# Kernel tuning notes

Measured on AMD Instinct MI355X. Metric: run time of the kernel, lower is better.

The kernel has to match this reference:

```python
import jax, jax.numpy as jnp
import numpy as np

EPS = 1e-8  # torch F.cosine_similarity norm clamp


def setup_inputs() -> dict:
    key = jax.random.key(0)
    k1, k2, k3, k4 = jax.random.split(key, 4)
    B, N, M, D, T = 8, 4096, 2048, 512, 2
    return {
        "features": jax.random.normal(k1, (B, N, D), dtype=jnp.float32),
        "text": jax.random.normal(k2, (T, M, D), dtype=jnp.float32),
        "W": jax.random.normal(k3, (D, D), dtype=jnp.float32) * 0.02,
        "b": jax.random.normal(k4, (D,), dtype=jnp.float32) * 0.02,
    }


def reference(features, text, W, b):
    # features: [B, N, D] (output of the extractor), text: [T, M, D]
    B, N, D = features.shape
    f1 = jnp.einsum("bnd,de->bne", features, W) + b  # linear_layer(features)
    t1 = text[1]  # [M, D]; expanded across batch (row 1 per original code)

    # cosine similarity over last dim without materializing [B, N, M, D]
    fn = f1 / jnp.maximum(jnp.linalg.norm(f1, axis=-1, keepdims=True), EPS)
    tn = t1 / jnp.maximum(jnp.linalg.norm(t1, axis=-1, keepdims=True), EPS)
    sim = jnp.einsum("bnd,md->bnm", fn, tn)  # [B, N, M]

    e = jnp.exp(sim)
    w = e / jnp.sum(e, axis=1, keepdims=True)  # normalize over N (dim=1)

    # features_t [B,D,N] @ w [B,N,M] -> [B,D,M] -> transpose -> [B,M,D]
    fm = jnp.einsum("bnd,bnm->bmd", features, w)

    t1b = jnp.broadcast_to(t1[None, :, :], (B,) + t1.shape)  # [B, M, D]
    combine_feature = jnp.concatenate([fm, t1b], axis=2)  # [B, M, 2D]
    return combine_feature
```

## Files before the change

### kernel.cpp

```cpp
#include <hip/hip_runtime.h>

#define B_SZ 8
#define N_SZ 4096
#define M_SZ 2048
#define D_SZ 512

typedef __attribute__((ext_vector_type(8))) short bf16x8;
typedef __attribute__((ext_vector_type(4))) float f32x4;
typedef __attribute__((address_space(1))) const void* gptr1;
typedef __attribute__((address_space(3))) void* lptr3;

__device__ __forceinline__ unsigned short f2bf(float x) {
    unsigned int u = __builtin_bit_cast(unsigned int, x);
    u += 0x7fffu + ((u >> 16) & 1u);
    return (unsigned short)(u >> 16);
}
__device__ __forceinline__ float bf2f(unsigned short u) {
    unsigned int x = ((unsigned int)u) << 16;
    return __builtin_bit_cast(float, x);
}

__device__ __forceinline__ void bt_mainloop(
    const unsigned short* __restrict__ A, const unsigned short* __restrict__ Bt,
    int lda, int ldb, int rowBase, int colBase, int K,
    unsigned short* As, unsigned short* Bs, f32x4 acc[4][4])
{
    const int tid  = threadIdx.x;
    const int lane = tid & 63;
    const int w    = tid >> 6;
    const int wr   = (w >> 1) * 64;
    const int wc   = (w & 1) * 64;
    const int lr   = lane & 15;
    const int kq   = lane >> 4;

    const int srow0 = w * 16 + (lane >> 2);
    const int skk   = (lane & 3) * 8;

    for (int k0 = 0; k0 < K; k0 += 32) {
#pragma unroll
        for (int j = 0; j < 2; ++j) {
            const unsigned short* ga = A  + (size_t)(rowBase + srow0 + j * 64) * lda + (k0 + skk);
            const unsigned short* gb = Bt + (size_t)(colBase + srow0 + j * 64) * ldb + (k0 + skk);
            __builtin_amdgcn_global_load_lds((gptr1)ga, (lptr3)(As + (j * 4 + w) * 512), 16, 0, 0);
            __builtin_amdgcn_global_load_lds((gptr1)gb, (lptr3)(Bs + (j * 4 + w) * 512), 16, 0, 0);
        }
        asm volatile("s_waitcnt vmcnt(0)" ::: "memory");
        __syncthreads();

        bf16x8 af[4], bq[4];
#pragma unroll
        for (int i = 0; i < 4; ++i) {
            af[i] = *(const bf16x8*)(As + (wr + i * 16 + lr) * 32 + kq * 8);
            bq[i] = *(const bf16x8*)(Bs + (wc + i * 16 + lr) * 32 + kq * 8);
        }
#pragma unroll
        for (int mi = 0; mi < 4; ++mi)
#pragma unroll
            for (int ni = 0; ni < 4; ++ni)
                acc[mi][ni] = __builtin_amdgcn_mfma_f32_16x16x32_bf16(af[mi], bq[ni], acc[mi][ni], 0, 0, 0);
        __syncthreads();
    }
}

__global__ __launch_bounds__(256) void prep_tn_k(
    const float* __restrict__ text, unsigned short* __restrict__ tn,
    float* __restrict__ out, float* __restrict__ L, float* __restrict__ SS)
{
    const int m = blockIdx.x;
    const int t = threadIdx.x;
    const float* t1 = text + (size_t)M_SZ * D_SZ;
    float2 v = ((const float2*)(t1 + (size_t)m * D_SZ))[t];
    float s = v.x * v.x + v.y * v.y;
#pragma unroll
    for (int off = 32; off > 0; off >>= 1) s += __shfl_down(s, off);
    __shared__ float partial[4];
    if ((t & 63) == 0) partial[t >> 6] = s;
    __syncthreads();
    float norm = sqrtf(partial[0] + partial[1] + partial[2] + partial[3]);
    norm = fmaxf(norm, 1e-8f);
    const float inv = 1.f / norm;
    ushort2 pk; pk.x = f2bf(v.x * inv); pk.y = f2bf(v.y * inv);
    ((ushort2*)(tn + (size_t)m * D_SZ))[t] = pk;
#pragma unroll
    for (int b = 0; b < B_SZ; ++b)
        ((float2*)(out + ((size_t)(b * M_SZ + m)) * (2 * D_SZ) + D_SZ))[t] = v;
    if (m < 64) L[m * 256 + t] = 0.f;
    if (m < 128) SS[m * 256 + t] = 0.f;
}

__global__ __launch_bounds__(256) void prep_w_k(
    const float* __restrict__ W, unsigned short* __restrict__ Wt)
{
    const int dt = blockIdx.x, et = blockIdx.y;
    const int t = threadIdx.x;
    __shared__ unsigned short tile[64][72];
    const int rr = t >> 4;
    const int cc = (t & 15) * 4;
#pragma unroll
    for (int p = 0; p < 4; ++p) {
        const int d = p * 16 + rr;
        const float4 v = *(const float4*)(W + (size_t)(dt * 64 + d) * D_SZ + et * 64 + cc);
        tile[d][cc] = f2bf(v.x); tile[d][cc + 1] = f2bf(v.y);
        tile[d][cc + 2] = f2bf(v.z); tile[d][cc + 3] = f2bf(v.w);
    }
    __syncthreads();
#pragma unroll
    for (int p = 0; p < 4; ++p) {
        const int e = p * 16 + rr;
        ushort4 pk;
        pk.x = tile[cc][e]; pk.y = tile[cc + 1][e]; pk.z = tile[cc + 2][e]; pk.w = tile[cc + 3][e];
        *(ushort4*)(Wt + (size_t)(et * 64 + e) * D_SZ + dt * 64 + cc) = pk;
    }
}

__global__ __launch_bounds__(256) void convert_feat_k(
    const float* __restrict__ feat, unsigned short* __restrict__ V,
    unsigned short* __restrict__ Vt)
{
    const int nt = blockIdx.x, dt = blockIdx.y, b = blockIdx.z;
    const int t = threadIdx.x;
    __shared__ unsigned short tile[64][72];
    const int rr = t >> 4;
    const int cc = (t & 15) * 4;
#pragma unroll
    for (int p = 0; p < 4; ++p) {
        const int r = p * 16 + rr;
        const size_t grow = (size_t)(b * N_SZ + nt * 64 + r);
        const float4 v = *(const float4*)(feat + grow * D_SZ + dt * 64 + cc);
        ushort4 pk; pk.x = f2bf(v.x); pk.y = f2bf(v.y); pk.z = f2bf(v.z); pk.w = f2bf(v.w);
        *(ushort4*)(V + grow * D_SZ + dt * 64 + cc) = pk;
        tile[r][cc] = pk.x; tile[r][cc + 1] = pk.y; tile[r][cc + 2] = pk.z; tile[r][cc + 3] = pk.w;
    }
    __syncthreads();
#pragma unroll
    for (int p = 0; p < 4; ++p) {
        const int d = p * 16 + rr;
        ushort4 pk;
        pk.x = tile[cc][d]; pk.y = tile[cc + 1][d]; pk.z = tile[cc + 2][d]; pk.w = tile[cc + 3][d];
        *(ushort4*)(Vt + ((size_t)(b * D_SZ + dt * 64 + d)) * N_SZ + nt * 64 + cc) = pk;
    }
}

__global__ __launch_bounds__(256) void gemm1_k(
    const unsigned short* __restrict__ V, const unsigned short* __restrict__ Wt,
    const float* __restrict__ bias, unsigned short* __restrict__ f1b,
    float* __restrict__ SS)
{
    __shared__ unsigned short As[128 * 32];
    __shared__ unsigned short Bs[128 * 32];
    f32x4 acc[4][4];
#pragma unroll
    for (int i = 0; i < 4; ++i)
#pragma unroll
        for (int j = 0; j < 4; ++j) acc[i][j] = (f32x4){0.f, 0.f, 0.f, 0.f};
    const int tid = threadIdx.x, lane = tid & 63, w = tid >> 6;
    const int wr = (w >> 1) * 64, wc = (w & 1) * 64, lr = lane & 15, kq = lane >> 4;

    const int rowBase = blockIdx.x * 128;
    const int colBase = blockIdx.y * 128;
    bt_mainloop(V, Wt, D_SZ, D_SZ, rowBase, colBase, D_SZ, As, Bs, acc);

#pragma unroll
    for (int mi = 0; mi < 4; ++mi) {
        const int r0 = rowBase + wr + mi * 16 + kq * 4;
        float s[4] = {0.f, 0.f, 0.f, 0.f};
#pragma unroll
        for (int ni = 0; ni < 4; ++ni) {
            const int c = colBase + wc + ni * 16 + lr;
            const float bv = bias[c];
#pragma unroll
            for (int r = 0; r < 4; ++r) {
                const float v = acc[mi][ni][r] + bv;
                f1b[(size_t)(r0 + r) * D_SZ + c] = f2bf(v);
                s[r] += v * v;
            }
        }
#pragma unroll
        for (int off = 1; off <= 8; off <<= 1)
#pragma unroll
            for (int r = 0; r < 4; ++r) s[r] += __shfl_xor(s[r], off);
        if (lr == 0) {
#pragma unroll
            for (int r = 0; r < 4; ++r) atomicAdd(&SS[r0 + r], s[r]);
        }
    }
}

__global__ __launch_bounds__(128) void normalize_k(
    const unsigned short* __restrict__ f1b, const float* __restrict__ SS,
    unsigned short* __restrict__ fn)
{
    const int row = blockIdx.x;
    const int t = threadIdx.x;
    const float norm = fmaxf(sqrtf(SS[row]), 1e-8f);
    const float inv = 1.f / norm;
    ushort4 v = ((const ushort4*)(f1b + (size_t)row * D_SZ))[t];
    ushort4 o;
    o.x = f2bf(bf2f(v.x) * inv); o.y = f2bf(bf2f(v.y) * inv);
    o.z = f2bf(bf2f(v.z) * inv); o.w = f2bf(bf2f(v.w) * inv);
    ((ushort4*)(fn + (size_t)row * D_SZ))[t] = o;
}

__global__ __launch_bounds__(256) void gemm2_k(
    const unsigned short* __restrict__ fn, const unsigned short* __restrict__ tn,
    unsigned short* __restrict__ E, float* __restrict__ L)
{
    __shared__ unsigned short smem[128 * 136];
    unsigned short* As = smem;
    unsigned short* Bs = smem + 4096;
    f32x4 acc[4][4];
#pragma unroll
    for (int i = 0; i < 4; ++i)
#pragma unroll
        for (int j = 0; j < 4; ++j) acc[i][j] = (f32x4){0.f, 0.f, 0.f, 0.f};
    const int tid = threadIdx.x, lane = tid & 63, w = tid >> 6;
    const int wr = (w >> 1) * 64, wc = (w & 1) * 64, lr = lane & 15, kq = lane >> 4;

    const int lin = blockIdx.x;
    const int xcd = lin & 7, slot = lin >> 3;
    const int mt = slot & 15;
    const int rt = (slot >> 4) * 8 + xcd;
    const int rowBase = rt * 128;
    const int colBase = mt * 128;

    bt_mainloop(fn, tn, D_SZ, D_SZ, rowBase, colBase, D_SZ, As, Bs, acc);

    const int b  = rowBase >> 12;
    const int nb = rowBase & 4095;
    unsigned short* Eb = E + (size_t)b * M_SZ * N_SZ;
    unsigned short* P = smem;

#pragma unroll
    for (int ni = 0; ni < 4; ++ni) {
        const int mm = wc + ni * 16 + lr;
        float p = 0.f;
#pragma unroll
        for (int mi = 0; mi < 4; ++mi) {
            const int nn0 = wr + mi * 16 + kq * 4;
            const float e0 = __expf(acc[mi][ni][0]);
            const float e1 = __expf(acc[mi][ni][1]);
            const float e2 = __expf(acc[mi][ni][2]);
            const float e3 = __expf(acc[mi][ni][3]);
            ushort4 pk; pk.x = f2bf(e0); pk.y = f2bf(e1); pk.z = f2bf(e2); pk.w = f2bf(e3);
            *(ushort4*)(P + mm * 136 + nn0) = pk;
            p += (e0 + e1) + (e2 + e3);
        }
        p += __shfl_down(p, 16);
        p += __shfl_down(p, 32);
        if (lane < 16) atomicAdd(&L[b * M_SZ + colBase + mm], p);
    }
    __syncthreads();

    const int tr = tid >> 4;
    const int tc = (tid & 15) * 8;
#pragma unroll
    for (int j = 0; j < 8; ++j) {
        const int mm = j * 16 + tr;
        bf16x8 v = *(const bf16x8*)(P + mm * 136 + tc);
        *(bf16x8*)(Eb + (size_t)(colBase + mm) * N_SZ + nb + tc) = v;
    }
}

__global__ __launch_bounds__(256) void gemm3_k(
    const unsigned short* __restrict__ E, const unsigned short* __restrict__ Vt,
    const float* __restrict__ L, float* __restrict__ out)
{
    __shared__ unsigned short As[128 * 32];
    __shared__ unsigned short Bs[128 * 32];
    f32x4 acc[4][4];
#pragma unroll
    for (int i = 0; i < 4; ++i)
#pragma unroll
        for (int j = 0; j < 4; ++j) acc[i][j] = (f32x4){0.f, 0.f, 0.f, 0.f};
    const int tid = threadIdx.x, lane = tid & 63, w = tid >> 6;
    const int wr = (w >> 1) * 64, wc = (w & 1) * 64, lr = lane & 15, kq = lane >> 4;

    const int b = blockIdx.z;
    const int rowBase = blockIdx.x * 128;
    const int colBase = blockIdx.y * 128;
    const unsigned short* Ab = E + (size_t)b * M_SZ * N_SZ;
    const unsigned short* Bb = Vt + (size_t)b * D_SZ * N_SZ;
    bt_mainloop(Ab, Bb, N_SZ, N_SZ, rowBase, colBase, N_SZ, As, Bs, acc);

#pragma unroll
    for (int mi = 0; mi < 4; ++mi) {
        const int r0 = rowBase + wr + mi * 16 + kq * 4;
        float invl[4];
#pragma unroll
        for (int r = 0; r < 4; ++r) invl[r] = 1.f / L[b * M_SZ + r0 + r];
#pragma unroll
        for (int ni = 0; ni < 4; ++ni) {
            const int d = colBase + wc + ni * 16 + lr;
#pragma unroll
            for (int r = 0; r < 4; ++r)
                out[((size_t)(b * M_SZ + r0 + r)) * (2 * D_SZ) + d] = acc[mi][ni][r] * invl[r];
        }
    }
}

extern "C" void kernel_launch(void* const* d_in, const int* in_sizes, int n_in,
                              void* d_out, int out_size, void* d_ws, size_t ws_size,
                              hipStream_t stream) {
    const float* features = (const float*)d_in[0];
    const float* text     = (const float*)d_in[1];
    const float* W        = (const float*)d_in[2];
    const float* bias     = (const float*)d_in[3];
    float* out = (float*)d_out;
    char* ws = (char*)d_ws;

    unsigned short* fn  = (unsigned short*)(ws + 0);
    unsigned short* tn  = (unsigned short*)(ws + 33554432);
    unsigned short* Wt  = (unsigned short*)(ws + 35651584);
    unsigned short* V   = (unsigned short*)(ws + 36175872);
    unsigned short* Vt  = (unsigned short*)(ws + 69730304);
    float*          L   = (float*)(ws + 103284736);
    float*          SS  = (float*)(ws + 103350272);
    unsigned short* E   = (unsigned short*)(ws + 103481344);
    unsigned short* f1b = (unsigned short*)(ws + 103481344);

    hipLaunchKernelGGL(prep_tn_k, dim3(M_SZ), dim3(256), 0, stream, text, tn, out, L, SS);
    hipLaunchKernelGGL(prep_w_k, dim3(8, 8), dim3(256), 0, stream, W, Wt);
    hipLaunchKernelGGL(convert_feat_k, dim3(64, 8, 8), dim3(256), 0, stream, features, V, Vt);
    hipLaunchKernelGGL(gemm1_k, dim3(256, 4), dim3(256), 0, stream, V, Wt, bias, f1b, SS);
    hipLaunchKernelGGL(normalize_k, dim3(32768), dim3(128), 0, stream, f1b, SS, fn);
    hipLaunchKernelGGL(gemm2_k, dim3(4096), dim3(256), 0, stream, fn, tn, E, L);
    hipLaunchKernelGGL(gemm3_k, dim3(16, 4, 8), dim3(256), 0, stream, E, Vt, L, out);
}
```

Before: 391.2 us.

## Rewrite similarity and weighted-sum GEMMs as 8-wave pipelined 256-wide tiles

Replaces the 4-wave 128x128 GEMM main loop with an 8-wave kernel. It uses 256-row tiles with BK=64 halves, XOR-swizzled LDS, and double-buffered async global-to-LDS loads that overlap each MFMA phase, with vmcnt waits and setprio. gemm2 now uses 256x256 tiles and a swizzled LDS transpose for its exp/bf16 epilogue. gemm3 uses 256x128 tiles over the full N reduction. The aim is more data reuse per tile and hidden load latency. The trade-off is one block per CU, far fewer blocks (256 for gemm3) and higher register pressure.

Result: faster. 367.8 us (-6.0%).

```diff
diff --git a/kernel.cpp b/kernel.cpp
--- a/kernel.cpp
+++ b/kernel.cpp
@@ -18,6 +18,13 @@
 __device__ __forceinline__ float bf2f(unsigned short u) {
     unsigned int x = ((unsigned int)u) << 16;
     return __builtin_bit_cast(float, x);
+}
+
+__device__ __forceinline__ void vmcnt0() { asm volatile("s_waitcnt vmcnt(0)" ::: "memory"); }
+__device__ __forceinline__ void vmcnt3() { asm volatile("s_waitcnt vmcnt(3)" ::: "memory"); }
+__device__ __forceinline__ void vmcnt4() { asm volatile("s_waitcnt vmcnt(4)" ::: "memory"); }
+template<int BN> __device__ __forceinline__ void vmcnt_steady() {
+    if constexpr (BN == 256) vmcnt4(); else vmcnt3();
 }
 
 __device__ __forceinline__ void bt_mainloop(
@@ -59,6 +66,91 @@
             for (int ni = 0; ni < 4; ++ni)
                 acc[mi][ni] = __builtin_amdgcn_mfma_f32_16x16x32_bf16(af[mi], bq[ni], acc[mi][ni], 0, 0, 0);
         __syncthreads();
+    }
+}
+
+template<int NROWS>
+__device__ __forceinline__ void stage_half(
+    const unsigned short* __restrict__ G, int ld, int grow0, int k0,
+    unsigned short* lds, int tid)
+{
+    const int w = tid >> 6, l = tid & 63;
+#pragma unroll
+    for (int c = 0; c < NROWS / 64; ++c) {
+        const int idx  = (c * 8 + w) * 64 + l;
+        const int row  = idx >> 3;
+        const int slot = (idx & 7) ^ (row & 7);
+        const unsigned short* ga = G + (size_t)(grow0 + row) * ld + (k0 + slot * 8);
+        __builtin_amdgcn_global_load_lds((gptr1)ga, (lptr3)(lds + (c * 8 + w) * 512), 16, 0, 0);
+    }
+}
+
+#define PHASE(BUF, QM, QN, STAGES, TAIL)                                              \
+  {                                                                                   \
+    const unsigned short* Ab = As + (BUF) * (256 * 64);                               \
+    const unsigned short* Bb = Bs + (BUF) * (BN * 64);                                \
+    bf16x8 af[4][2], bq[NF2][2];                                                      \
+    _Pragma("unroll") for (int mi = 0; mi < 4; ++mi)                                  \
+      _Pragma("unroll") for (int ks = 0; ks < 2; ++ks) {                              \
+        const int row = (QM) * 128 + wrow + mi * 16 + lr;                             \
+        af[mi][ks] = *(const bf16x8*)(Ab + row * 64 + (((ks * 4 + kq) ^ (row & 7)) * 8)); \
+      }                                                                               \
+    _Pragma("unroll") for (int ni = 0; ni < NF2; ++ni)                                \
+      _Pragma("unroll") for (int ks = 0; ks < 2; ++ks) {                              \
+        const int row = (QN) * (BN / 2) + wcol + ni * 16 + lr;                        \
+        bq[ni][ks] = *(const bf16x8*)(Bb + row * 64 + (((ks * 4 + kq) ^ (row & 7)) * 8)); \
+      }                                                                               \
+    STAGES;                                                                           \
+    __builtin_amdgcn_s_barrier();                                                     \
+    __builtin_amdgcn_s_setprio(1);                                                    \
+    _Pragma("unroll") for (int mi = 0; mi < 4; ++mi)                                  \
+      _Pragma("unroll") for (int ni = 0; ni < NF2; ++ni)                              \
+        _Pragma("unroll") for (int ks = 0; ks < 2; ++ks)                              \
+          acc[(QM) * 4 + mi][(QN) * NF2 + ni] = __builtin_amdgcn_mfma_f32_16x16x32_bf16( \
+              af[mi][ks], bq[ni][ks], acc[(QM) * 4 + mi][(QN) * NF2 + ni], 0, 0, 0);  \
+    __builtin_amdgcn_s_setprio(0);                                                    \
+    TAIL;                                                                             \
+    __builtin_amdgcn_s_barrier();                                                     \
+  }
+
+template<int BN>
+__device__ __forceinline__ void mainloop8(
+    const unsigned short* __restrict__ A, const unsigned short* __restrict__ Bt,
+    int lda, int ldb, int rowBase, int colBase, int K,
+    unsigned short* As, unsigned short* Bs, f32x4 (&acc)[8][BN / 64])
+{
+    constexpr int NF2  = BN / 128;
+    constexpr int BNH  = BN / 2;
+    constexpr int ABUF = 256 * 64, AH = 128 * 64;
+    constexpr int BBUF = BN * 64,  BH = BNH * 64;
+    const int tid = threadIdx.x, lane = tid & 63, w = tid >> 6;
+    const int wrow = (w >> 2) * 64;
+    const int wcol = (w & 3) * (BN / 8);
+    const int lr = lane & 15, kq = lane >> 4;
+    const int niter = K >> 7;
+
+    stage_half<128>(A,  lda, rowBase,       0,  As,        tid);
+    stage_half<BNH>(Bt, ldb, colBase,       0,  Bs,        tid);
+    stage_half<128>(A,  lda, rowBase + 128, 0,  As + AH,   tid);
+    stage_half<BNH>(Bt, ldb, colBase + BNH, 0,  Bs + BH,   tid);
+    stage_half<128>(A,  lda, rowBase,       64, As + ABUF, tid);
+    stage_half<BNH>(Bt, ldb, colBase,       64, Bs + BBUF, tid);
+    vmcnt_steady<BN>();
+    __builtin_amdgcn_s_barrier();
+
+    for (int I = 0; I < niter; ++I) {
+        const bool nl = (I + 1 < niter);
+        const int ke = I << 7;
+        PHASE(0, 0, 0, { stage_half<128>(A,  lda, rowBase + 128, ke + 64,  As + ABUF + AH, tid); }, {});
+        PHASE(0, 0, 1, { stage_half<BNH>(Bt, ldb, colBase + BNH, ke + 64,  Bs + BBUF + BH, tid); }, {});
+        PHASE(0, 1, 0, { if (nl) stage_half<128>(A,  lda, rowBase,       ke + 128, As,      tid); }, {});
+        PHASE(0, 1, 1, { if (nl) stage_half<BNH>(Bt, ldb, colBase,       ke + 128, Bs,      tid); },
+                       { if (nl) vmcnt_steady<BN>(); else vmcnt0(); });
+        PHASE(1, 0, 0, { if (nl) stage_half<128>(A,  lda, rowBase + 128, ke + 128, As + AH, tid); }, {});
+        PHASE(1, 0, 1, { if (nl) stage_half<BNH>(Bt, ldb, colBase + BNH, ke + 128, Bs + BH, tid); }, {});
+        PHASE(1, 1, 0, { if (nl) stage_half<128>(A,  lda, rowBase,       ke + 192, As + ABUF, tid); }, {});
+        PHASE(1, 1, 1, { if (nl) stage_half<BNH>(Bt, ldb, colBase,       ke + 192, Bs + BBUF, tid); },
+                       { if (nl) vmcnt_steady<BN>(); else vmcnt0(); });
     }
 }
 
@@ -201,99 +293,113 @@
     ((ushort4*)(fn + (size_t)row * D_SZ))[t] = o;
 }
 
-__global__ __launch_bounds__(256) void gemm2_k(
+__global__ __launch_bounds__(512, 1) void gemm2_k8(
     const unsigned short* __restrict__ fn, const unsigned short* __restrict__ tn,
     unsigned short* __restrict__ E, float* __restrict__ L)
 {
-    __shared__ unsigned short smem[128 * 136];
+    __shared__ unsigned short smem[65536];
     unsigned short* As = smem;
-    unsigned short* Bs = smem + 4096;
-    f32x4 acc[4][4];
-#pragma unroll
-    for (int i = 0; i < 4; ++i)
+    unsigned short* Bs = smem + 32768;
+    f32x4 acc[8][4];
+#pragma unroll
+    for (int i = 0; i < 8; ++i)
 #pragma unroll
         for (int j = 0; j < 4; ++j) acc[i][j] = (f32x4){0.f, 0.f, 0.f, 0.f};
-    const int tid = threadIdx.x, lane = tid & 63, w = tid >> 6;
-    const int wr = (w >> 1) * 64, wc = (w & 1) * 64, lr = lane & 15, kq = lane >> 4;
 
     const int lin = blockIdx.x;
     const int xcd = lin & 7, slot = lin >> 3;
-    const int mt = slot & 15;
-    const int rt = (slot >> 4) * 8 + xcd;
-    const int rowBase = rt * 128;
-    const int colBase = mt * 128;
-
-    bt_mainloop(fn, tn, D_SZ, D_SZ, rowBase, colBase, D_SZ, As, Bs, acc);
-
-    const int b  = rowBase >> 12;
-    const int nb = rowBase & 4095;
-    unsigned short* Eb = E + (size_t)b * M_SZ * N_SZ;
+    const int mt = slot & 7;
+    const int rt = (slot >> 3) * 8 + xcd;
+    const int rowBase = rt * 256;
+    const int colBase = mt * 256;
+
+    mainloop8<256>(fn, tn, D_SZ, D_SZ, rowBase, colBase, D_SZ, As, Bs, acc);
+    __syncthreads();
+
+    const int tid = threadIdx.x, lane = tid & 63, w = tid >> 6;
+    const int wrow = (w >> 2) * 64, wcol = (w & 3) * 32;
+    const int lr = lane & 15, kq = lane >> 4;
+    const int b = rowBase >> 12;
+    const int nb0 = rowBase & 4095;
+
     unsigned short* P = smem;
-
-#pragma unroll
-    for (int ni = 0; ni < 4; ++ni) {
-        const int mm = wc + ni * 16 + lr;
-        float p = 0.f;
-#pragma unroll
-        for (int mi = 0; mi < 4; ++mi) {
-            const int nn0 = wr + mi * 16 + kq * 4;
-            const float e0 = __expf(acc[mi][ni][0]);
-            const float e1 = __expf(acc[mi][ni][1]);
-            const float e2 = __expf(acc[mi][ni][2]);
-            const float e3 = __expf(acc[mi][ni][3]);
+    float ps[4] = {0.f, 0.f, 0.f, 0.f};
+#pragma unroll
+    for (int a = 0; a < 8; ++a) {
+        const int n0 = (a >> 2) * 128 + wrow + (a & 3) * 16 + kq * 4;
+#pragma unroll
+        for (int j = 0; j < 4; ++j) {
+            const int m = (j >> 1) * 128 + wcol + (j & 1) * 16 + lr;
+            const float e0 = __expf(acc[a][j][0]);
+            const float e1 = __expf(acc[a][j][1]);
+            const float e2 = __expf(acc[a][j][2]);
+            const float e3 = __expf(acc[a][j][3]);
             ushort4 pk; pk.x = f2bf(e0); pk.y = f2bf(e1); pk.z = f2bf(e2); pk.w = f2bf(e3);
-            *(ushort4*)(P + mm * 136 + nn0) = pk;
-            p += (e0 + e1) + (e2 + e3);
-        }
+            *(ushort4*)(P + m * 256 + (((n0 >> 3) ^ (m & 7)) * 8) + (n0 & 7)) = pk;
+            ps[j] += (e0 + e1) + (e2 + e3);
+        }
+    }
+#pragma unroll
+    for (int j = 0; j < 4; ++j) {
+        float p = ps[j];
         p += __shfl_down(p, 16);
         p += __shfl_down(p, 32);
-        if (lane < 16) atomicAdd(&L[b * M_SZ + colBase + mm], p);
+        const int m = (j >> 1) * 128 + wcol + (j & 1) * 16 + lr;
+        if (lane < 16) atomicAdd(&L[b * M_SZ + colBase + m], p);
     }
     __syncthreads();
 
-    const int tr = tid >> 4;
-    const int tc = (tid & 15) * 8;
-#pragma unroll
-    for (int j = 0; j < 8; ++j) {
-        const int mm = j * 16 + tr;
-        bf16x8 v = *(const bf16x8*)(P + mm * 136 + tc);
-        *(bf16x8*)(Eb + (size_t)(colBase + mm) * N_SZ + nb + tc) = v;
-    }
-}
-
-__global__ __launch_bounds__(256) void gemm3_k(
+    unsigned short* Eb = E + (size_t)b * M_SZ * N_SZ;
+#pragma unroll
+    for (int c = 0; c < 16; ++c) {
+        const int rm = c * 16 + (tid >> 5);
+        const int ns = tid & 31;
+        bf16x8 v = *(const bf16x8*)(P + rm * 256 + ((ns ^ (rm & 7)) * 8));
+        *(bf16x8*)(Eb + (size_t)(colBase + rm) * N_SZ + nb0 + ns * 8) = v;
+    }
+}
+
+__global__ __launch_bounds__(512, 1) void gemm3_k8(
     const unsigned short* __restrict__ E, const unsigned short* __restrict__ Vt,
     const float* __restrict__ L, float* __restrict__ out)
 {
-    __shared__ unsigned short As[128 * 32];
-    __shared__ unsigned short Bs[128 * 32];
-    f32x4 acc[4][4];
-#pragma unroll
-    for (int i = 0; i < 4; ++i)
-#pragma unroll
-        for (int j = 0; j < 4; ++j) acc[i][j] = (f32x4){0.f, 0.f, 0.f, 0.f};
-    const int tid = threadIdx.x, lane = tid & 63, w = tid >> 6;
-    const int wr = (w >> 1) * 64, wc = (w & 1) * 64, lr = lane & 15, kq = lane >> 4;
-
-    const int b = blockIdx.z;
-    const int rowBase = blockIdx.x * 128;
-    const int colBase = blockIdx.y * 128;
+    __shared__ unsigned short smem[49152];
+    unsigned short* As = smem;
+    unsigned short* Bs = smem + 32768;
+    f32x4 acc[8][2];
+#pragma unroll
+    for (int i = 0; i < 8; ++i)
+#pragma unroll
+        for (int j = 0; j < 2; ++j) acc[i][j] = (f32x4){0.f, 0.f, 0.f, 0.f};
+
+    const int lin = blockIdx.x;
+    const int mtile = lin & 7;
+    const int slot = lin >> 3;
+    const int dt = slot & 3;
+    const int b = slot >> 2;
+    const int rowBase = mtile * 256;
+    const int colBase = dt * 128;
+
     const unsigned short* Ab = E + (size_t)b * M_SZ * N_SZ;
     const unsigned short* Bb = Vt + (size_t)b * D_SZ * N_SZ;
-    bt_mainloop(Ab, Bb, N_SZ, N_SZ, rowBase, colBase, N_SZ, As, Bs, acc);
-
-#pragma unroll
-    for (int mi = 0; mi < 4; ++mi) {
-        const int r0 = rowBase + wr + mi * 16 + kq * 4;
+    mainloop8<128>(Ab, Bb, N_SZ, N_SZ, rowBase, colBase, N_SZ, As, Bs, acc);
+
+    const int tid = threadIdx.x, lane = tid & 63, w = tid >> 6;
+    const int wrow = (w >> 2) * 64, wcol = (w & 3) * 16;
+    const int lr = lane & 15, kq = lane >> 4;
+
+#pragma unroll
+    for (int a = 0; a < 8; ++a) {
+        const int r0 = rowBase + (a >> 2) * 128 + wrow + (a & 3) * 16 + kq * 4;
         float invl[4];
 #pragma unroll
         for (int r = 0; r < 4; ++r) invl[r] = 1.f / L[b * M_SZ + r0 + r];
 #pragma unroll
-        for (int ni = 0; ni < 4; ++ni) {
-            const int d = colBase + wc + ni * 16 + lr;
+        for (int j = 0; j < 2; ++j) {
+            const int d = colBase + j * 64 + wcol + lr;
 #pragma unroll
             for (int r = 0; r < 4; ++r)
-                out[((size_t)(b * M_SZ + r0 + r)) * (2 * D_SZ) + d] = acc[mi][ni][r] * invl[r];
+                out[((size_t)(b * M_SZ + r0 + r)) * (2 * D_SZ) + d] = acc[a][j][r] * invl[r];
         }
     }
 }
@@ -323,6 +429,6 @@
     hipLaunchKernelGGL(convert_feat_k, dim3(64, 8, 8), dim3(256), 0, stream, features, V, Vt);
     hipLaunchKernelGGL(gemm1_k, dim3(256, 4), dim3(256), 0, stream, V, Wt, bias, f1b, SS);
     hipLaunchKernelGGL(normalize_k, dim3(32768), dim3(128), 0, stream, f1b, SS, fn);
-    hipLaunchKernelGGL(gemm2_k, dim3(4096), dim3(256), 0, stream, fn, tn, E, L);
-    hipLaunchKernelGGL(gemm3_k, dim3(16, 4, 8), dim3(256), 0, stream, E, Vt, L, out);
-}
+    hipLaunchKernelGGL(gemm2_k8, dim3(1024), dim3(512), 0, stream, fn, tn, E, L);
+    hipLaunchKernelGGL(gemm3_k8, dim3(256), dim3(512), 0, stream, E, Vt, L, out);
+}
```
